# Kernel optimization log

Measured on AMD Instinct MI355X. Metric: run time of the kernel, lower is better.

Reference implementation:

```python
import jax, jax.numpy as jnp
import numpy as np

KP_EXTENT = 1.2  # influence radius of each kernel point (init arg KP_extent)
SHADOW_COORD = 1e6  # shadow point coordinate for padding (as in original KPConv)


def setup_inputs() -> dict:
    key = jax.random.key(0)
    k1, k2, k3, k4, k5, k6 = jax.random.split(key, 6)
    N, Ns, H, K, Cin, Cout = 20000, 20000, 40, 15, 128, 128
    q_pts = jax.random.uniform(k1, (N, 3), dtype=jnp.float32)
    s_pts = jax.random.uniform(k2, (Ns, 3), dtype=jnp.float32)
    neighb_inds = jax.random.randint(k3, (N, H), 0, Ns, dtype=jnp.int32)
    x = jax.random.normal(k4, (Ns, Cin), dtype=jnp.float32)
    # kernel point positions inside the sphere (stand-in for load_kernels output)
    kernel_points = jax.random.normal(k5, (K, 3), dtype=jnp.float32) * 0.5
    kernel_points = kernel_points.at[0].set(0.0)  # fixed='center'
    weights = jax.random.normal(k6, (K, Cin, Cout), dtype=jnp.float32) * (1.0 / np.sqrt(Cin))
    return {"q_pts": q_pts, "s_pts": s_pts, "neighb_inds": neighb_inds,
            "x": x, "kernel_points": kernel_points, "weights": weights}


def reference(q_pts, s_pts, neighb_inds, x, kernel_points, weights):
    # Pad support points with a far-away shadow point and features with a zero row,
    # so out-of-range neighbor index Ns contributes nothing (original KPConv trick).
    s_pad = jnp.concatenate([s_pts, jnp.full((1, s_pts.shape[1]), SHADOW_COORD, s_pts.dtype)], axis=0)
    x_pad = jnp.concatenate([x, jnp.zeros((1, x.shape[1]), x.dtype)], axis=0)

    # Gather neighbor coords, center on query points: [N, H, 3]
    neighbors = s_pad[neighb_inds] - q_pts[:, None, :]

    # Squared distance to every kernel point: [N, H, K]
    diff = neighbors[:, :, None, :] - kernel_points[None, None, :, :]
    sq_dist = jnp.sum(diff * diff, axis=-1)

    # Linear influence weights, aggregation_mode='sum': [N, K, H]
    all_weights = jnp.clip(1.0 - jnp.sqrt(sq_dist) / KP_EXTENT, 0.0, None)
    all_weights = jnp.swapaxes(all_weights, 1, 2)

    # Gather neighbor features: [N, H, Cin]
    neighb_x = x_pad[neighb_inds]

    # Influence-weighted aggregation over neighbors: [N, K, Cin]
    weighted = jnp.einsum('nkh,nhc->nkc', all_weights, neighb_x)

    # Per-kernel-point linear maps, summed over kernel points: [N, Cout]
    out = jnp.einsum('nkc,kcd->nd', weighted, weights)
    return out
```

## Files before the change

### kernel.cpp

```cpp
#include <hip/hip_runtime.h>

#define KP   15
#define HN   40
#define CIN  128
#define COUT 128
#define KDIM (KP*CIN)
#define KP_EXT_INV (1.0f/1.2f)

typedef __bf16 bf16x8 __attribute__((ext_vector_type(8)));
typedef float  f32x4  __attribute__((ext_vector_type(4)));

__device__ inline void async_copy16(const void* g, void* lds) {
    __builtin_amdgcn_global_load_lds(
        (const __attribute__((address_space(1))) unsigned int*)g,
        (__attribute__((address_space(3))) unsigned int*)lds, 16, 0, 0);
}

__global__ __launch_bounds__(256)
void convert_w(const float* __restrict__ W, __bf16* __restrict__ Bt) {
    const int e  = blockIdx.x * 256 + threadIdx.x;
    const int d  = e / KDIM;
    const int kc = e - d * KDIM;
    Bt[e] = (__bf16)W[(size_t)kc * COUT + d];
}

#define XSTR 40

__global__ __launch_bounds__(256, 2)
void kpconv_aggregate(const float* __restrict__ q_pts,
                      const float* __restrict__ s_pts,
                      const int*   __restrict__ nb,
                      const float* __restrict__ x,
                      const float* __restrict__ kpts,
                      __bf16* __restrict__ wsA,
                      int N, int Ns)
{
    __shared__ __align__(16) __bf16 sXt[4][CIN][XSTR];
    __shared__ __align__(16) float4 s_nd[4][HN];
    __shared__ __align__(16) int    s_idx[4][HN];

    const int t  = threadIdx.x;
    const int wv = t >> 6;
    const int l  = t & 63;
    const int n  = blockIdx.x * 4 + wv;

    if (l < HN) {
        int idx = nb[n*HN + l];
        float dx, dy, dz;
        if (idx >= 0 && idx < Ns) {
            dx = s_pts[idx*3+0] - q_pts[n*3+0];
            dy = s_pts[idx*3+1] - q_pts[n*3+1];
            dz = s_pts[idx*3+2] - q_pts[n*3+2];
        } else { idx = 0; dx = dy = dz = 2.0e6f; }
        s_idx[wv][l] = idx;
        s_nd[wv][l]  = make_float4(dx, dy, dz, 0.f);
    }
    __syncthreads();

    const int m = l & 15;
    const int q = l >> 4;
    float kx = 0.f, ky = 0.f, kz = 0.f;
    if (m < KP) { kx = kpts[m*3+0]; ky = kpts[m*3+1]; kz = kpts[m*3+2]; }

    bf16x8 wfrag[2];
    #pragma unroll
    for (int ks = 0; ks < 2; ++ks) {
        #pragma unroll
        for (int j = 0; j < 8; ++j) {
            const int h = ks*32 + q*8 + j;
            float w = 0.f;
            if (m < KP && h < HN) {
                float4 nd = s_nd[wv][h];
                float dx = nd.x - kx, dy = nd.y - ky, dz = nd.z - kz;
                float d = sqrtf(dx*dx + dy*dy + dz*dz);
                w = fmaxf(1.0f - d * KP_EXT_INV, 0.f);
            }
            wfrag[ks][j] = (__bf16)w;
        }
    }

    f32x4 acc[8];
    #pragma unroll
    for (int nt = 0; nt < 8; ++nt) acc[nt] = (f32x4){0.f, 0.f, 0.f, 0.f};

    for (int ks = 0; ks < 2; ++ks) {
        #pragma unroll
        for (int pass = 0; pass < 2; ++pass) {
            const int c = pass*64 + l;
            const float* xc = x + c;
            #pragma unroll
            for (int hb = 0; hb < 4; ++hb) {
                const int hg0 = ks*32 + hb*8;
                bf16x8 vv;
                if (hg0 < HN) {
                    int4 ia = *(const int4*)&s_idx[wv][hg0];
                    int4 ib = *(const int4*)&s_idx[wv][hg0 + 4];
                    vv[0] = (__bf16)xc[(size_t)ia.x * CIN];
                    vv[1] = (__bf16)xc[(size_t)ia.y * CIN];
                    vv[2] = (__bf16)xc[(size_t)ia.z * CIN];
                    vv[3] = (__bf16)xc[(size_t)ia.w * CIN];
                    vv[4] = (__bf16)xc[(size_t)ib.x * CIN];
                    vv[5] = (__bf16)xc[(size_t)ib.y * CIN];
                    vv[6] = (__bf16)xc[(size_t)ib.z * CIN];
                    vv[7] = (__bf16)xc[(size_t)ib.w * CIN];
                } else {
                    #pragma unroll
                    for (int j = 0; j < 8; ++j) vv[j] = (__bf16)0.f;
                }
                *(bf16x8*)&sXt[wv][c][hb*8] = vv;
            }
        }
        __syncthreads();

        #pragma unroll
        for (int nt = 0; nt < 8; ++nt) {
            const int c = nt*16 + m;
            bf16x8 bfrag = *(const bf16x8*)&sXt[wv][c][q*8];
            acc[nt] = __builtin_amdgcn_mfma_f32_16x16x32_bf16(
                          wfrag[ks], bfrag, acc[nt], 0, 0, 0);
        }
        __syncthreads();
    }

    #pragma unroll
    for (int nt = 0; nt < 8; ++nt) {
        #pragma unroll
        for (int r = 0; r < 4; ++r) {
            const int row = q*4 + r;
            if (row < KP) {
                wsA[(size_t)n*KDIM + row*CIN + nt*16 + m] = (__bf16)acc[nt][r];
            }
        }
    }
}

#define BM 32
#define BK 64

__global__ __launch_bounds__(256, 2)
void kpconv_gemm(const __bf16* __restrict__ A,
                 const __bf16* __restrict__ Bt,
                 float* __restrict__ out, int M)
{
    __shared__ __align__(16) __bf16 sA[BM*BK];
    __shared__ __align__(16) __bf16 sB[COUT*BK];

    const int t     = threadIdx.x;
    const int wv    = t >> 6;
    const int l     = t & 63;
    const int mlane = l & 15;
    const int q     = l >> 4;
    const int m0    = blockIdx.x * BM;

    const int ra = t >> 3;
    const int ca = t & 7;
    const int sw = (ca ^ (ra & 7)) * 8;
    const __bf16* gA = A  + (size_t)(m0 + ra) * KDIM + sw;
    const __bf16* gB0 = Bt + (size_t)(0*32 + ra) * KDIM + sw;
    const __bf16* gB1 = Bt + (size_t)(1*32 + ra) * KDIM + sw;
    const __bf16* gB2 = Bt + (size_t)(2*32 + ra) * KDIM + sw;
    const __bf16* gB3 = Bt + (size_t)(3*32 + ra) * KDIM + sw;

    __bf16* dA = &sA[wv*512];
    __bf16* dB0 = &sB[0*2048 + wv*512];
    __bf16* dB1 = &sB[1*2048 + wv*512];
    __bf16* dB2 = &sB[2*2048 + wv*512];
    __bf16* dB3 = &sB[3*2048 + wv*512];

    f32x4 acc[2][2];
    #pragma unroll
    for (int i = 0; i < 2; ++i)
        #pragma unroll
        for (int j = 0; j < 2; ++j) acc[i][j] = (f32x4){0.f,0.f,0.f,0.f};

    for (int k0 = 0; k0 < KDIM; k0 += BK) {
        async_copy16(gA  + k0, dA);
        async_copy16(gB0 + k0, dB0);
        async_copy16(gB1 + k0, dB1);
        async_copy16(gB2 + k0, dB2);
        async_copy16(gB3 + k0, dB3);
        __syncthreads();

        #pragma unroll
        for (int ks = 0; ks < 2; ++ks) {
            bf16x8 af[2], bf[2];
            #pragma unroll
            for (int mt = 0; mt < 2; ++mt) {
                const int row = mt*16 + mlane;
                const int ch  = (ks*4 + q) ^ (mlane & 7);
                af[mt] = *(const bf16x8*)&sA[row*BK + ch*8];
            }
            #pragma unroll
            for (int j = 0; j < 2; ++j) {
                const int row = (wv*2 + j)*16 + mlane;
                const int ch  = (ks*4 + q) ^ (mlane & 7);
                bf[j] = *(const bf16x8*)&sB[row*BK + ch*8];
            }
            #pragma unroll
            for (int mt = 0; mt < 2; ++mt)
                #pragma unroll
                for (int j = 0; j < 2; ++j)
                    acc[mt][j] = __builtin_amdgcn_mfma_f32_16x16x32_bf16(
                                     af[mt], bf[j], acc[mt][j], 0, 0, 0);
        }
        __syncthreads();
    }

    #pragma unroll
    for (int mt = 0; mt < 2; ++mt)
        #pragma unroll
        for (int j = 0; j < 2; ++j)
            #pragma unroll
            for (int r = 0; r < 4; ++r)
                out[(size_t)(m0 + mt*16 + q*4 + r)*COUT + (wv*2+j)*16 + mlane]
                    = acc[mt][j][r];
}

#define TM 8
#define WSTR (KP*CIN + 4)

__global__ __launch_bounds__(256, 2)
void kpconv_fused(const float* __restrict__ q_pts,
                  const float* __restrict__ s_pts,
                  const int*   __restrict__ nb,
                  const float* __restrict__ x,
                  const float* __restrict__ kpts,
                  const float* __restrict__ W,
                  float* __restrict__ out,
                  int N, int Ns)
{
    __shared__ float s_kp[KP*3];
    __shared__ float s_nd2[HN*3];
    __shared__ int   s_idx2[HN];
    __shared__ float s_w[KP][HN];
    __shared__ float s_wt[TM*WSTR];

    const int t  = threadIdx.x;
    const int n0 = (int)blockIdx.x * TM;
    if (t < KP*3) s_kp[t] = kpts[t];
    const int c = t & (CIN-1);
    const int g = t >> 7;

    for (int m = 0; m < TM; ++m) {
        const int n = n0 + m;
        if (t < HN) {
            float dx = 1e6f, dy = 1e6f, dz = 1e6f;
            int idx = 0;
            if (n < N) {
                idx = nb[n*HN + t];
                if (idx >= 0 && idx < Ns) {
                    dx = s_pts[idx*3+0] - q_pts[n*3+0];
                    dy = s_pts[idx*3+1] - q_pts[n*3+1];
                    dz = s_pts[idx*3+2] - q_pts[n*3+2];
                } else idx = 0;
            }
            s_idx2[t] = idx;
            s_nd2[t*3+0] = dx; s_nd2[t*3+1] = dy; s_nd2[t*3+2] = dz;
        }
        __syncthreads();
        for (int task = t; task < KP*HN; task += 256) {
            const int k = task / HN;
            const int h = task - k*HN;
            const float dx = s_nd2[h*3+0] - s_kp[k*3+0];
            const float dy = s_nd2[h*3+1] - s_kp[k*3+1];
            const float dz = s_nd2[h*3+2] - s_kp[k*3+2];
            s_w[k][h] = fmaxf(1.0f - sqrtf(dx*dx+dy*dy+dz*dz)*KP_EXT_INV, 0.0f);
        }
        __syncthreads();
        float facc[8];
        #pragma unroll
        for (int j = 0; j < 8; ++j) facc[j] = 0.0f;
        #pragma unroll 8
        for (int h = 0; h < HN; ++h) {
            const float xv = x[s_idx2[h]*CIN + c];
            #pragma unroll
            for (int j = 0; j < 8; ++j) {
                const int k = g + 2*j;
                if (k < KP) facc[j] += s_w[k][h] * xv;
            }
        }
        #pragma unroll
        for (int j = 0; j < 8; ++j) {
            const int k = g + 2*j;
            if (k < KP) s_wt[m*WSTR + k*CIN + c] = facc[j];
        }
        __syncthreads();
    }

    const int m3 = t >> 5;
    const int d0 = (t & 31) * 4;
    const float* wm = &s_wt[m3*WSTR];
    float ax = 0.f, ay = 0.f, az = 0.f, aw = 0.f;
    #pragma unroll 4
    for (int kc = 0; kc < KP*CIN; ++kc) {
        const float  wvv = wm[kc];
        const float4 wr = *(const float4*)&W[kc*COUT + d0];
        ax += wvv * wr.x; ay += wvv * wr.y; az += wvv * wr.z; aw += wvv * wr.w;
    }
    const int n = n0 + m3;
    if (n < N) {
        float4 o; o.x = ax; o.y = ay; o.z = az; o.w = aw;
        *(float4*)&out[n*COUT + d0] = o;
    }
}

extern "C" void kernel_launch(void* const* d_in, const int* in_sizes, int n_in,
                              void* d_out, int out_size, void* d_ws, size_t ws_size,
                              hipStream_t stream) {
    const float* q_pts = (const float*)d_in[0];
    const float* s_pts = (const float*)d_in[1];
    const int*   nb    = (const int*)  d_in[2];
    const float* x     = (const float*)d_in[3];
    const float* kpts  = (const float*)d_in[4];
    const float* W     = (const float*)d_in[5];
    float* out = (float*)d_out;

    const int N  = in_sizes[0] / 3;
    const int Ns = in_sizes[1] / 3;

    const size_t needA = (size_t)N * KDIM * sizeof(__bf16);
    const size_t needB = (size_t)COUT * KDIM * sizeof(__bf16);

    if (ws_size >= needA + needB && (N % 4) == 0 && (N % BM) == 0) {
        __bf16* wsA = (__bf16*)d_ws;
        __bf16* wsB = (__bf16*)((char*)d_ws + needA);
        hipLaunchKernelGGL(convert_w, dim3((COUT*KDIM)/256), dim3(256), 0, stream,
                           W, wsB);
        hipLaunchKernelGGL(kpconv_aggregate, dim3(N/4), dim3(256), 0, stream,
                           q_pts, s_pts, nb, x, kpts, wsA, N, Ns);
        hipLaunchKernelGGL(kpconv_gemm, dim3(N/BM), dim3(256), 0, stream,
                           wsA, wsB, out, N);
    } else {
        const int grid = (N + TM - 1) / TM;
        hipLaunchKernelGGL(kpconv_fused, dim3(grid), dim3(256), 0, stream,
                           q_pts, s_pts, nb, x, kpts, W, out, N, Ns);
    }
}
```

Baseline: 164.1 us.

## Pre-convert features to bf16 and use vectorized row gathers with swizzled LDS

Adds a prep kernel that converts x to bf16 and transposes W through LDS with coalesced loads, replacing the scalar convert_w. The aggregate kernel now gathers 16-byte contiguous bf16 row chunks per neighbor instead of strided scalar fp32 loads, and packs pairs into a swizzled LDS layout for the MFMA B operand. Occupancy is raised to 4 blocks per CU. The GEMM tile K depth doubles to 128 with a 16-way XOR swizzle, halving loop iterations and barriers. The cost is an extra pass over x and more workspace.

```diff
diff --git a/kernel.cpp b/kernel.cpp
--- a/kernel.cpp
+++ b/kernel.cpp
@@ -17,27 +17,60 @@
 }
 
 __global__ __launch_bounds__(256)
-void convert_w(const float* __restrict__ W, __bf16* __restrict__ Bt) {
-    const int e  = blockIdx.x * 256 + threadIdx.x;
-    const int d  = e / KDIM;
-    const int kc = e - d * KDIM;
-    Bt[e] = (__bf16)W[(size_t)kc * COUT + d];
-}
-
-#define XSTR 40
-
-__global__ __launch_bounds__(256, 2)
+void kpconv_prep(const float* __restrict__ x, const float* __restrict__ W,
+                 __bf16* __restrict__ xb, __bf16* __restrict__ Wt,
+                 int nx_elems, int nxB)
+{
+    __shared__ float sW[32][133];
+    const int b = blockIdx.x;
+    const int t = threadIdx.x;
+
+    if (b < nxB) {
+        const int e0 = (b*256 + t) * 8;
+        if (e0 + 8 <= nx_elems) {
+            const float4 f0 = *(const float4*)(x + e0);
+            const float4 f1 = *(const float4*)(x + e0 + 4);
+            bf16x8 v;
+            v[0]=(__bf16)f0.x; v[1]=(__bf16)f0.y; v[2]=(__bf16)f0.z; v[3]=(__bf16)f0.w;
+            v[4]=(__bf16)f1.x; v[5]=(__bf16)f1.y; v[6]=(__bf16)f1.z; v[7]=(__bf16)f1.w;
+            *(bf16x8*)(xb + e0) = v;
+        } else {
+            for (int e = e0; e < nx_elems; ++e) xb[e] = (__bf16)x[e];
+        }
+    } else {
+        const int kc0 = (b - nxB) * 32;
+        #pragma unroll
+        for (int i = 0; i < 4; ++i) {
+            const int off = t*4 + i*1024;
+            const int r = off >> 7, c = off & 127;
+            const float4 f = *(const float4*)(W + (size_t)(kc0 + r)*COUT + c);
+            sW[r][c+0]=f.x; sW[r][c+1]=f.y; sW[r][c+2]=f.z; sW[r][c+3]=f.w;
+        }
+        __syncthreads();
+        #pragma unroll
+        for (int i = 0; i < 2; ++i) {
+            const int id = t + i*256;
+            const int d  = id >> 2, ch = id & 3;
+            bf16x8 v;
+            #pragma unroll
+            for (int j = 0; j < 8; ++j) v[j] = (__bf16)sW[ch*8 + j][d];
+            *(bf16x8*)(Wt + (size_t)d*KDIM + kc0 + ch*8) = v;
+        }
+    }
+}
+
+__global__ __launch_bounds__(256, 4)
 void kpconv_aggregate(const float* __restrict__ q_pts,
                       const float* __restrict__ s_pts,
                       const int*   __restrict__ nb,
-                      const float* __restrict__ x,
+                      const __bf16* __restrict__ xb,
                       const float* __restrict__ kpts,
                       __bf16* __restrict__ wsA,
                       int N, int Ns)
 {
-    __shared__ __align__(16) __bf16 sXt[4][CIN][XSTR];
+    __shared__ __align__(16) __bf16 sXt[4][4][128][8];
     __shared__ __align__(16) float4 s_nd[4][HN];
-    __shared__ __align__(16) int    s_idx[4][HN];
+    __shared__ int                  s_idx[4][HN];
 
     const int t  = threadIdx.x;
     const int wv = t >> 6;
@@ -72,8 +105,7 @@
             if (m < KP && h < HN) {
                 float4 nd = s_nd[wv][h];
                 float dx = nd.x - kx, dy = nd.y - ky, dz = nd.z - kz;
-                float d = sqrtf(dx*dx + dy*dy + dz*dz);
-                w = fmaxf(1.0f - d * KP_EXT_INV, 0.f);
+                w = fmaxf(1.0f - sqrtf(dx*dx + dy*dy + dz*dz) * KP_EXT_INV, 0.f);
             }
             wfrag[ks][j] = (__bf16)w;
         }
@@ -83,39 +115,36 @@
     #pragma unroll
     for (int nt = 0; nt < 8; ++nt) acc[nt] = (f32x4){0.f, 0.f, 0.f, 0.f};
 
+    const int c8 = l & 15;
+
     for (int ks = 0; ks < 2; ++ks) {
-        #pragma unroll
-        for (int pass = 0; pass < 2; ++pass) {
-            const int c = pass*64 + l;
-            const float* xc = x + c;
-            #pragma unroll
-            for (int hb = 0; hb < 4; ++hb) {
-                const int hg0 = ks*32 + hb*8;
-                bf16x8 vv;
-                if (hg0 < HN) {
-                    int4 ia = *(const int4*)&s_idx[wv][hg0];
-                    int4 ib = *(const int4*)&s_idx[wv][hg0 + 4];
-                    vv[0] = (__bf16)xc[(size_t)ia.x * CIN];
-                    vv[1] = (__bf16)xc[(size_t)ia.y * CIN];
-                    vv[2] = (__bf16)xc[(size_t)ia.z * CIN];
-                    vv[3] = (__bf16)xc[(size_t)ia.w * CIN];
-                    vv[4] = (__bf16)xc[(size_t)ib.x * CIN];
-                    vv[5] = (__bf16)xc[(size_t)ib.y * CIN];
-                    vv[6] = (__bf16)xc[(size_t)ib.z * CIN];
-                    vv[7] = (__bf16)xc[(size_t)ib.w * CIN];
-                } else {
-                    #pragma unroll
-                    for (int j = 0; j < 8; ++j) vv[j] = (__bf16)0.f;
-                }
-                *(bf16x8*)&sXt[wv][c][hb*8] = vv;
+        const int hpBeg = ks ? 16 : 0;
+        const int hpEnd = ks ? 20 : 16;
+        for (int hp = hpBeg + (l >> 4); hp < hpEnd; hp += 4) {
+            const int h0 = 2*hp;
+            const uint4 a = *(const uint4*)(xb + (size_t)s_idx[wv][h0  ]*CIN + c8*8);
+            const uint4 bb= *(const uint4*)(xb + (size_t)s_idx[wv][h0+1]*CIN + c8*8);
+            const unsigned int av[4] = {a.x, a.y, a.z, a.w};
+            const unsigned int bv[4] = {bb.x, bb.y, bb.z, bb.w};
+            const int hl = h0 - ks*32;
+            const int hc = hl >> 3;
+            const int dw = hp & 3;
+            unsigned int* plane = (unsigned int*)&sXt[wv][hc][0][0];
+            #pragma unroll
+            for (int j = 0; j < 8; ++j) {
+                const unsigned int lo = (av[j>>1] >> ((j&1)*16)) & 0xFFFFu;
+                const unsigned int hi = (bv[j>>1] >> ((j&1)*16)) & 0xFFFFu;
+                const int p = c8*8 + (j ^ (c8 & 7));
+                plane[p*4 + dw] = lo | (hi << 16);
             }
         }
         __syncthreads();
 
         #pragma unroll
         for (int nt = 0; nt < 8; ++nt) {
-            const int c = nt*16 + m;
-            bf16x8 bfrag = *(const bf16x8*)&sXt[wv][c][q*8];
+            const int cc = nt*16 + m;
+            const int p  = (cc & ~7) | ((cc & 7) ^ ((cc >> 3) & 7));
+            bf16x8 bfrag = *(const bf16x8*)&sXt[wv][q][p][0];
             acc[nt] = __builtin_amdgcn_mfma_f32_16x16x32_bf16(
                           wfrag[ks], bfrag, acc[nt], 0, 0, 0);
         }
@@ -127,15 +156,14 @@
         #pragma unroll
         for (int r = 0; r < 4; ++r) {
             const int row = q*4 + r;
-            if (row < KP) {
+            if (row < KP)
                 wsA[(size_t)n*KDIM + row*CIN + nt*16 + m] = (__bf16)acc[nt][r];
-            }
         }
     }
 }
 
 #define BM 32
-#define BK 64
+#define BK 128
 
 __global__ __launch_bounds__(256, 2)
 void kpconv_gemm(const __bf16* __restrict__ A,
@@ -152,20 +180,8 @@
     const int q     = l >> 4;
     const int m0    = blockIdx.x * BM;
 
-    const int ra = t >> 3;
-    const int ca = t & 7;
-    const int sw = (ca ^ (ra & 7)) * 8;
-    const __bf16* gA = A  + (size_t)(m0 + ra) * KDIM + sw;
-    const __bf16* gB0 = Bt + (size_t)(0*32 + ra) * KDIM + sw;
-    const __bf16* gB1 = Bt + (size_t)(1*32 + ra) * KDIM + sw;
-    const __bf16* gB2 = Bt + (size_t)(2*32 + ra) * KDIM + sw;
-    const __bf16* gB3 = Bt + (size_t)(3*32 + ra) * KDIM + sw;
-
-    __bf16* dA = &sA[wv*512];
-    __bf16* dB0 = &sB[0*2048 + wv*512];
-    __bf16* dB1 = &sB[1*2048 + wv*512];
-    __bf16* dB2 = &sB[2*2048 + wv*512];
-    __bf16* dB3 = &sB[3*2048 + wv*512];
+    const int rA = t >> 4;
+    const int pA = t & 15;
 
     f32x4 acc[2][2];
     #pragma unroll
@@ -174,34 +190,43 @@
         for (int j = 0; j < 2; ++j) acc[i][j] = (f32x4){0.f,0.f,0.f,0.f};
 
     for (int k0 = 0; k0 < KDIM; k0 += BK) {
-        async_copy16(gA  + k0, dA);
-        async_copy16(gB0 + k0, dB0);
-        async_copy16(gB1 + k0, dB1);
-        async_copy16(gB2 + k0, dB2);
-        async_copy16(gB3 + k0, dB3);
-        __syncthreads();
-
-        #pragma unroll
-        for (int ks = 0; ks < 2; ++ks) {
-            bf16x8 af[2], bf[2];
+        #pragma unroll
+        for (int pass = 0; pass < 2; ++pass) {
+            const int r  = rA + pass*16;
+            const int ch = pA ^ (r & 15);
+            async_copy16(A + (size_t)(m0 + r)*KDIM + k0 + ch*8,
+                         (char*)sA + pass*4096 + wv*1024 + l*16);
+        }
+        #pragma unroll
+        for (int pass = 0; pass < 8; ++pass) {
+            const int r  = rA + pass*16;
+            const int ch = pA ^ (r & 15);
+            async_copy16(Bt + (size_t)r*KDIM + k0 + ch*8,
+                         (char*)sB + pass*4096 + wv*1024 + l*16);
+        }
+        __syncthreads();
+
+        #pragma unroll
+        for (int ksi = 0; ksi < 4; ++ksi) {
+            bf16x8 af[2], bfr[2];
             #pragma unroll
             for (int mt = 0; mt < 2; ++mt) {
                 const int row = mt*16 + mlane;
-                const int ch  = (ks*4 + q) ^ (mlane & 7);
-                af[mt] = *(const bf16x8*)&sA[row*BK + ch*8];
+                const int p   = (ksi*4 + q) ^ (row & 15);
+                af[mt] = *(const bf16x8*)&sA[row*BK + p*8];
             }
             #pragma unroll
             for (int j = 0; j < 2; ++j) {
                 const int row = (wv*2 + j)*16 + mlane;
-                const int ch  = (ks*4 + q) ^ (mlane & 7);
-                bf[j] = *(const bf16x8*)&sB[row*BK + ch*8];
+                const int p   = (ksi*4 + q) ^ (row & 15);
+                bfr[j] = *(const bf16x8*)&sB[row*BK + p*8];
             }
             #pragma unroll
             for (int mt = 0; mt < 2; ++mt)
                 #pragma unroll
                 for (int j = 0; j < 2; ++j)
                     acc[mt][j] = __builtin_amdgcn_mfma_f32_16x16x32_bf16(
-                                     af[mt], bf[j], acc[mt][j], 0, 0, 0);
+                                     af[mt], bfr[j], acc[mt][j], 0, 0, 0);
         }
         __syncthreads();
     }
@@ -317,17 +342,24 @@
 
     const int N  = in_sizes[0] / 3;
     const int Ns = in_sizes[1] / 3;
+    const int nx = in_sizes[3];
 
     const size_t needA = (size_t)N * KDIM * sizeof(__bf16);
     const size_t needB = (size_t)COUT * KDIM * sizeof(__bf16);
-
-    if (ws_size >= needA + needB && (N % 4) == 0 && (N % BM) == 0) {
+    const size_t needX = (size_t)nx * sizeof(__bf16);
+
+    if (ws_size >= needA + needB + needX && (N % 4) == 0 && (N % BM) == 0
+        && (KDIM % 32) == 0) {
         __bf16* wsA = (__bf16*)d_ws;
         __bf16* wsB = (__bf16*)((char*)d_ws + needA);
-        hipLaunchKernelGGL(convert_w, dim3((COUT*KDIM)/256), dim3(256), 0, stream,
-                           W, wsB);
+        __bf16* wsX = (__bf16*)((char*)d_ws + needA + needB);
+
+        const int nxB = (nx/8 + 255) / 256;
+        const int nwB = KDIM / 32;
+        hipLaunchKernelGGL(kpconv_prep, dim3(nxB + nwB), dim3(256), 0, stream,
+                           x, W, wsX, wsB, nx, nxB);
         hipLaunchKernelGGL(kpconv_aggregate, dim3(N/4), dim3(256), 0, stream,
-                           q_pts, s_pts, nb, x, kpts, wsA, N, Ns);
+                           q_pts, s_pts, nb, wsX, kpts, wsA, N, Ns);
         hipLaunchKernelGGL(kpconv_gemm, dim3(N/BM), dim3(256), 0, stream,
                            wsA, wsB, out, N);
     } else {
```

Result: faster. 146.1 us (-11.0%).
